# Performance work log

Measured on AMD Instinct MI355X. Metric: run time of the kernel, lower is better.

The kernel has to match this reference:

```python
import jax, jax.numpy as jnp
import numpy as np

M, N, D, P = 1024, 4096, 128, 2048
H = N // D  # 32
L = 4096   # cache length


def setup_inputs() -> dict:
    key = jax.random.key(0)
    ks = jax.random.split(key, 6)
    # scales keep the naive (non max-subtracted) exp-softmax in fp32 range
    X = jax.random.normal(ks[0], (M, N), dtype=jnp.float32) * 0.5
    W_q = jax.random.normal(ks[1], (N, N), dtype=jnp.float32) * 0.01
    W_k = jax.random.normal(ks[2], (N, N), dtype=jnp.float32) * 0.01
    W_v = jax.random.normal(ks[3], (N, N), dtype=jnp.float32) * 0.01
    cache_K = jax.random.normal(ks[4], (H, L, D), dtype=jnp.float32) * 0.1
    cache_V = jax.random.normal(ks[5], (H, L, D), dtype=jnp.float32) * 0.1
    return {"X": X, "W_q": W_q, "W_k": W_k, "W_v": W_v,
            "cache_K": cache_K, "cache_V": cache_V}


def reference(X, W_q, W_k, W_v, cache_K, cache_V):
    # fused QKV projection: [M, N] @ [N, 3N]
    W_qkv = jnp.concatenate([W_q, W_k, W_v], axis=1)
    qkv = X @ W_qkv
    q, k, v = jnp.split(qkv, 3, axis=-1)
    q = q.reshape(M, H, D).transpose(1, 0, 2)  # [H, M, D]
    k = k.reshape(M, H, D).transpose(1, 0, 2)  # [H, M, D]
    v = v.reshape(M, H, D).transpose(1, 0, 2)  # [H, M, D]
    # KV-cache write at position P
    k_cache = jax.lax.dynamic_update_slice(cache_K, k, (0, P, 0))  # [H, L, D]
    v_cache = jax.lax.dynamic_update_slice(cache_V, v, (0, P, 0))
    # naive (no max-subtraction) exp softmax attention over the full cache
    scores = jnp.einsum('hmd,hld->hml', q, k_cache)  # [H, M, L]
    scores_exp = jnp.exp(scores)
    weights = scores_exp / jnp.sum(scores_exp, axis=-1, keepdims=True)
    output = jnp.einsum('hml,hld->hmd', weights, v_cache)  # [H, M, D]
    return output.transpose(1, 0, 2).reshape(M, H * D)
```

## Files before the change

### kernel.cpp

```cpp
#include <hip/hip_runtime.h>

#define MM 1024
#define NN 4096
#define DD 128
#define HH 32
#define LL 4096
#define PP 2048

typedef __attribute__((ext_vector_type(8))) short short8;
typedef __attribute__((ext_vector_type(4))) float f32x4;

__device__ __forceinline__ ushort f2bf(float f) {
  unsigned u = __builtin_bit_cast(unsigned, f);
  u += 0x7fffu + ((u >> 16) & 1u);
  return (ushort)(u >> 16);
}

__device__ __forceinline__ void gl_lds16(const void* g, void* l) {
  __builtin_amdgcn_global_load_lds(
      (const __attribute__((address_space(1))) void*)g,
      (__attribute__((address_space(3))) void*)l, 16, 0, 0);
}

__global__ __launch_bounds__(256) void convert_kernel(
    const float* __restrict__ src, ushort* __restrict__ dst, int n8) {
  int i = blockIdx.x * 256 + threadIdx.x;
  if (i >= n8) return;
  const float4* s = (const float4*)src + (size_t)i * 2;
  float4 a = s[0], b = s[1];
  union { ushort s[8]; uint4 v; } pk;
  pk.s[0] = f2bf(a.x); pk.s[1] = f2bf(a.y);
  pk.s[2] = f2bf(a.z); pk.s[3] = f2bf(a.w);
  pk.s[4] = f2bf(b.x); pk.s[5] = f2bf(b.y);
  pk.s[6] = f2bf(b.z); pk.s[7] = f2bf(b.w);
  ((uint4*)dst)[i] = pk.v;
}

__global__ __launch_bounds__(256) void transpose_w_kernel(
    const float* __restrict__ W0, const float* __restrict__ W1,
    const float* __restrict__ W2, ushort* __restrict__ Wt) {
  __shared__ __align__(16) ushort tile[64][72];
  int z = blockIdx.z;
  const float* W = (z == 0) ? W0 : ((z == 1) ? W1 : W2);
  ushort* out = Wt + (size_t)z * NN * NN;
  int r0 = blockIdx.x * 64, c0 = blockIdx.y * 64;
  int t = threadIdx.x;
#pragma unroll
  for (int i = 0; i < 4; ++i) {
    int c = i * 256 + t;
    int r = c >> 4, cc = (c & 15) * 4;
    float4 v = *(const float4*)(W + (size_t)(r0 + r) * NN + c0 + cc);
    tile[r][cc + 0] = f2bf(v.x);
    tile[r][cc + 1] = f2bf(v.y);
    tile[r][cc + 2] = f2bf(v.z);
    tile[r][cc + 3] = f2bf(v.w);
  }
  __syncthreads();
#pragma unroll
  for (int i = 0; i < 2; ++i) {
    int c = i * 256 + t;
    int j = c >> 3, kk = (c & 7) * 8;
    union { ushort s[8]; uint4 v; } pk;
#pragma unroll
    for (int u = 0; u < 8; ++u) pk.s[u] = tile[kk + u][j];
    *(uint4*)(out + (size_t)(c0 + j) * NN + r0 + kk) = pk.v;
  }
}

__global__ __launch_bounds__(256) void transpose_v_kernel(
    const float* __restrict__ cacheV, const ushort* __restrict__ v_new,
    ushort* __restrict__ Vt) {
  __shared__ __align__(16) ushort tile[64][72];
  int l0 = blockIdx.x * 64, d0 = blockIdx.y * 64, h = blockIdx.z;
  int t = threadIdx.x;
  bool isnew = (l0 >= PP && l0 < PP + MM);
  if (isnew) {
    const ushort* src = v_new + (size_t)(l0 - PP) * NN + h * DD + d0;
#pragma unroll
    for (int i = 0; i < 2; ++i) {
      int c = i * 256 + t;
      int r = c >> 3, cc = (c & 7) * 8;
      *(uint4*)&tile[r][cc] = *(const uint4*)(src + (size_t)r * NN + cc);
    }
  } else {
    const float* src = cacheV + ((size_t)h * LL + l0) * DD + d0;
#pragma unroll
    for (int i = 0; i < 4; ++i) {
      int c = i * 256 + t;
      int r = c >> 4, cc = (c & 15) * 4;
      float4 v = *(const float4*)(src + (size_t)r * DD + cc);
      tile[r][cc + 0] = f2bf(v.x);
      tile[r][cc + 1] = f2bf(v.y);
      tile[r][cc + 2] = f2bf(v.z);
      tile[r][cc + 3] = f2bf(v.w);
    }
  }
  __syncthreads();
#pragma unroll
  for (int i = 0; i < 2; ++i) {
    int c = i * 256 + t;
    int j = c >> 3, kk = (c & 7) * 8;
    union { ushort s[8]; uint4 v; } pk;
#pragma unroll
    for (int u = 0; u < 8; ++u) pk.s[u] = tile[kk + u][j];
    *(uint4*)(Vt + ((size_t)(h * DD + d0 + j)) * LL + l0 + kk) = pk.v;
  }
}

__global__ __launch_bounds__(256) void qkv_gemm_kernel(
    const ushort* __restrict__ X, const ushort* __restrict__ Wt,
    ushort* __restrict__ q_ws, ushort* __restrict__ k_ws,
    ushort* __restrict__ v_ws) {
  __shared__ __align__(16) ushort Alds[128 * 64];
  __shared__ __align__(16) ushort Blds[128 * 64];
  int t = threadIdx.x;
  int lane = t & 63, quad = lane >> 4, l15 = lane & 15;
  int wv = t >> 6, wm = wv >> 1, wn = wv & 1;
  int m0 = blockIdx.x * 128;
  int wsel = blockIdx.y >> 5;
  int col0 = (blockIdx.y & 31) * 128;
  const ushort* Wsrc = Wt + (size_t)wsel * NN * NN + (size_t)col0 * NN;
  ushort* dst = (wsel == 0) ? q_ws : ((wsel == 1) ? k_ws : v_ws);

  int wuni = __builtin_amdgcn_readfirstlane(t & 192);

  const ushort* aG[4];
  const ushort* bG[4];
  unsigned ldsb[4];
#pragma unroll
  for (int i = 0; i < 4; ++i) {
    int c = i * 256 + t;
    int row = c >> 3, g = (c & 7) ^ (row & 7);
    aG[i] = X + (size_t)(m0 + row) * NN + g * 8;
    bG[i] = Wsrc + (size_t)row * NN + g * 8;
    ldsb[i] = (unsigned)(i * 256 + wuni) * 16u;
  }
  unsigned aAddr[4][2], bAddr[4][2];
#pragma unroll
  for (int mb = 0; mb < 4; ++mb)
#pragma unroll
    for (int s = 0; s < 2; ++s) {
      int row = wm * 64 + mb * 16 + l15;
      int g = s * 4 + quad;
      aAddr[mb][s] = (unsigned)(row * 128 + ((g ^ (row & 7)) * 16));
    }
#pragma unroll
  for (int nb = 0; nb < 4; ++nb)
#pragma unroll
    for (int s = 0; s < 2; ++s) {
      int row = wn * 64 + nb * 16 + l15;
      int g = s * 4 + quad;
      bAddr[nb][s] = (unsigned)(row * 128 + ((g ^ (row & 7)) * 16));
    }

  f32x4 acc[4][4];
#pragma unroll
  for (int mb = 0; mb < 4; ++mb)
#pragma unroll
    for (int nb = 0; nb < 4; ++nb) acc[mb][nb] = (f32x4){0.f, 0.f, 0.f, 0.f};

  for (int kt = 0; kt < 64; ++kt) {
#pragma unroll
    for (int i = 0; i < 4; ++i) gl_lds16(aG[i], (char*)Alds + ldsb[i]);
#pragma unroll
    for (int i = 0; i < 4; ++i) gl_lds16(bG[i], (char*)Blds + ldsb[i]);
#pragma unroll
    for (int i = 0; i < 4; ++i) { aG[i] += 64; bG[i] += 64; }
    __syncthreads();
#pragma unroll
    for (int s = 0; s < 2; ++s) {
      short8 af[4], bf[4];
#pragma unroll
      for (int mb = 0; mb < 4; ++mb)
        af[mb] = *(const short8*)((const char*)Alds + aAddr[mb][s]);
#pragma unroll
      for (int nb = 0; nb < 4; ++nb)
        bf[nb] = *(const short8*)((const char*)Blds + bAddr[nb][s]);
#pragma unroll
      for (int mb = 0; mb < 4; ++mb)
#pragma unroll
        for (int nb = 0; nb < 4; ++nb)
          acc[mb][nb] = __builtin_amdgcn_mfma_f32_16x16x32_bf16(
              af[mb], bf[nb], acc[mb][nb], 0, 0, 0);
    }
    __syncthreads();
  }

#pragma unroll
  for (int mb = 0; mb < 4; ++mb)
#pragma unroll
    for (int nb = 0; nb < 4; ++nb)
#pragma unroll
      for (int r = 0; r < 4; ++r) {
        int row = m0 + wm * 64 + mb * 16 + quad * 4 + r;
        int col = col0 + wn * 64 + nb * 16 + l15;
        dst[(size_t)row * NN + col] = f2bf(acc[mb][nb][r]);
      }
}

__global__ __launch_bounds__(256) void attn_kernel(
    const ushort* __restrict__ q_ws, const ushort* __restrict__ k_ws,
    const ushort* __restrict__ Kb, const ushort* __restrict__ Vt,
    float* __restrict__ out) {
  __shared__ __align__(16) char smem[42240];
  float* denlds = (float*)(smem + 41984);
  float* Olds = (float*)smem;

  int t = threadIdx.x;
  int lane = t & 63, quad = lane >> 4, l15 = lane & 15;
  int wv = t >> 6;
  int h = blockIdx.y, m0 = blockIdx.x * 64;
  int wuni = __builtin_amdgcn_readfirstlane(t & 192);

  short8 qf[4];
  {
    const ushort* qrow =
        q_ws + (size_t)(m0 + wv * 16 + l15) * NN + h * DD + quad * 8;
#pragma unroll
    for (int s = 0; s < 4; ++s) qf[s] = *(const short8*)(qrow + s * 32);
  }

  int kRow[4], kOff[4];
  unsigned kLb[4];
  const ushort* vG[4];
  unsigned vLb[4];
#pragma unroll
  for (int i = 0; i < 4; ++i) {
    int c = i * 256 + t;
    int krow = c >> 4, kg = (c & 15) ^ (krow & 15);
    kRow[i] = krow; kOff[i] = kg * 8;
    kLb[i] = (unsigned)(i * 256 + wuni) * 16u;
    int vrow = c >> 3, vg = (c & 7) ^ (vrow & 7);
    vG[i] = Vt + ((size_t)(h * DD + vrow)) * LL + vg * 8;
    vLb[i] = 16384u + (unsigned)(i * 256 + wuni) * 16u;
  }
  unsigned kAddr[4][4], vAddr[2][2], pAddr[2][4];
#pragma unroll
  for (int lb = 0; lb < 4; ++lb)
#pragma unroll
    for (int ds = 0; ds < 4; ++ds) {
      int l = lb * 16 + l15, g = ds * 4 + quad;
      kAddr[lb][ds] = (unsigned)(l * 256 + ((g ^ l15) * 16));
    }
#pragma unroll
  for (int ls = 0; ls < 2; ++ls)
#pragma unroll
    for (int db = 0; db < 2; ++db) {
      int d = wv * 32 + db * 16 + l15, g = ls * 4 + quad;
      vAddr[ls][db] = 16384u + (unsigned)(d * 128 + ((g ^ (l15 & 7)) * 16));
    }
#pragma unroll
  for (int ls = 0; ls < 2; ++ls)
#pragma unroll
    for (int mb = 0; mb < 4; ++mb)
      pAddr[ls][mb] =
          32768u + (unsigned)((mb * 16 + l15) * 144 + ls * 64 + quad * 16);

  f32x4 Oacc[2][4];
#pragma unroll
  for (int db = 0; db < 2; ++db)
#pragma unroll
    for (int mb = 0; mb < 4; ++mb) Oacc[db][mb] = (f32x4){0.f, 0.f, 0.f, 0.f};
  float denp[4] = {0.f, 0.f, 0.f, 0.f};

  for (int lt = 0; lt < 64; ++lt) {
    int l0 = lt * 64;
    const ushort* ksrc;
    size_t kstride;
    if (l0 >= PP && l0 < PP + MM) {
      ksrc = k_ws + (size_t)(l0 - PP) * NN + h * DD;
      kstride = NN;
    } else {
      ksrc = Kb + ((size_t)h * LL + l0) * DD;
      kstride = DD;
    }
    __syncthreads();
#pragma unroll
    for (int i = 0; i < 4; ++i)
      gl_lds16(ksrc + (size_t)kRow[i] * kstride + kOff[i], smem + kLb[i]);
#pragma unroll
    for (int i = 0; i < 4; ++i) {
      gl_lds16(vG[i], smem + vLb[i]);
      vG[i] += 64;
    }
    __syncthreads();

#pragma unroll
    for (int lb = 0; lb < 4; ++lb) {
      f32x4 s = (f32x4){0.f, 0.f, 0.f, 0.f};
#pragma unroll
      for (int ds = 0; ds < 4; ++ds) {
        short8 bk = *(const short8*)(smem + kAddr[lb][ds]);
        s = __builtin_amdgcn_mfma_f32_16x16x32_bf16(qf[ds], bk, s, 0, 0, 0);
      }
#pragma unroll
      for (int r = 0; r < 4; ++r) {
        float e = __expf(s[r]);
        denp[r] += e;
        *(ushort*)(smem + 32768 + (wv * 16 + quad * 4 + r) * 144 +
                   (lb * 16 + l15) * 2) = f2bf(e);
      }
    }
    __syncthreads();

#pragma unroll
    for (int ls = 0; ls < 2; ++ls) {
      short8 av0 = *(const short8*)(smem + vAddr[ls][0]);
      short8 av1 = *(const short8*)(smem + vAddr[ls][1]);
#pragma unroll
      for (int mb = 0; mb < 4; ++mb) {
        short8 bp = *(const short8*)(smem + pAddr[ls][mb]);
        Oacc[0][mb] =
            __builtin_amdgcn_mfma_f32_16x16x32_bf16(av0, bp, Oacc[0][mb], 0, 0, 0);
        Oacc[1][mb] =
            __builtin_amdgcn_mfma_f32_16x16x32_bf16(av1, bp, Oacc[1][mb], 0, 0, 0);
      }
    }
  }

  __syncthreads();
#pragma unroll
  for (int r = 0; r < 4; ++r) {
    float v = denp[r];
    v += __shfl_xor(v, 1);
    v += __shfl_xor(v, 2);
    v += __shfl_xor(v, 4);
    v += __shfl_xor(v, 8);
    denp[r] = v;
  }
  if (l15 == 0) {
#pragma unroll
    for (int r = 0; r < 4; ++r) denlds[wv * 16 + quad * 4 + r] = denp[r];
  }
  __syncthreads();

#pragma unroll
  for (int mb = 0; mb < 4; ++mb) {
    float inv = 1.0f / denlds[mb * 16 + l15];
#pragma unroll
    for (int db = 0; db < 2; ++db)
#pragma unroll
      for (int r = 0; r < 4; ++r) {
        int d = wv * 32 + db * 16 + quad * 4 + r;
        Olds[(mb * 16 + l15) * 136 + d] = Oacc[db][mb][r] * inv;
      }
  }
  __syncthreads();
  {
    int m = t >> 2, c0 = (t & 3) * 32;
    float* orow = out + (size_t)(m0 + m) * NN + h * DD + c0;
#pragma unroll
    for (int j = 0; j < 32; j += 4) {
      float4 v;
      v.x = Olds[m * 136 + c0 + j + 0];
      v.y = Olds[m * 136 + c0 + j + 1];
      v.z = Olds[m * 136 + c0 + j + 2];
      v.w = Olds[m * 136 + c0 + j + 3];
      *(float4*)(orow + j) = v;
    }
  }
}

extern "C" void kernel_launch(void* const* d_in, const int* in_sizes, int n_in,
                              void* d_out, int out_size, void* d_ws,
                              size_t ws_size, hipStream_t stream) {
  const float* X = (const float*)d_in[0];
  const float* Wq = (const float*)d_in[1];
  const float* Wk = (const float*)d_in[2];
  const float* Wv = (const float*)d_in[3];
  const float* cK = (const float*)d_in[4];
  const float* cV = (const float*)d_in[5];
  float* out = (float*)d_out;
  char* wsb = (char*)d_ws;

  ushort* Wt = (ushort*)wsb;
  ushort* Kb = (ushort*)wsb;
  ushort* Vt = (ushort*)(wsb + 33554432);
  ushort* Xb = (ushort*)(wsb + 100663296);
  ushort* q_ws = (ushort*)(wsb + 109051904);
  ushort* k_ws = (ushort*)(wsb + 117440512);
  ushort* v_ws = (ushort*)(wsb + 125829120);

  convert_kernel<<<2048, 256, 0, stream>>>(X, Xb, MM * NN / 8);
  transpose_w_kernel<<<dim3(64, 64, 3), 256, 0, stream>>>(Wq, Wk, Wv, Wt);
  qkv_gemm_kernel<<<dim3(8, 96), 256, 0, stream>>>(Xb, Wt, q_ws, k_ws, v_ws);
  convert_kernel<<<8192, 256, 0, stream>>>(cK, Kb, HH * LL * DD / 8);
  transpose_v_kernel<<<dim3(64, 2, 32), 256, 0, stream>>>(cV, v_ws, Vt);
  attn_kernel<<<dim3(16, 32), 256, 0, stream>>>(q_ws, k_ws, Kb, Vt, out);
}
```

Measured before the change: 566.2 us.

## Double-buffer K tiles with manual vmcnt waits and remap attention block indices

Adds a second LDS buffer for K so the next tile's K load is issued while the current tile is being computed. Replaces __syncthreads with explicit s_waitcnt vmcnt counts plus s_barrier, and raises wave priority around the MFMA sections. It also swizzles the block-to-(head, m-tile) mapping so concurrently scheduled blocks share heads differently, aiming for better cache locality. LDS use grows, which may lower occupancy, and hand-counted vmcnt values are fragile if the compiler reorders memory ops.

Result: no change. 564.6 us, median of 2 (-0.3%).

```diff
diff --git a/kernel.cpp b/kernel.cpp
--- a/kernel.cpp
+++ b/kernel.cpp
@@ -202,14 +202,17 @@
     const ushort* __restrict__ q_ws, const ushort* __restrict__ k_ws,
     const ushort* __restrict__ Kb, const ushort* __restrict__ Vt,
     float* __restrict__ out) {
-  __shared__ __align__(16) char smem[42240];
-  float* denlds = (float*)(smem + 41984);
+  __shared__ __align__(16) char smem[58624];
+  float* denlds = (float*)(smem + 58368);
   float* Olds = (float*)smem;
 
   int t = threadIdx.x;
   int lane = t & 63, quad = lane >> 4, l15 = lane & 15;
   int wv = t >> 6;
-  int h = blockIdx.y, m0 = blockIdx.x * 64;
+  int flat = (int)(blockIdx.y * 16 + blockIdx.x);
+  int swz = ((flat & 7) << 6) | (flat >> 3);
+  int m0 = (swz & 15) * 64;
+  int h = swz >> 4;
   int wuni = __builtin_amdgcn_readfirstlane(t & 192);
 
   short8 qf[4];
@@ -232,7 +235,7 @@
     kLb[i] = (unsigned)(i * 256 + wuni) * 16u;
     int vrow = c >> 3, vg = (c & 7) ^ (vrow & 7);
     vG[i] = Vt + ((size_t)(h * DD + vrow)) * LL + vg * 8;
-    vLb[i] = 16384u + (unsigned)(i * 256 + wuni) * 16u;
+    vLb[i] = 32768u + (unsigned)(i * 256 + wuni) * 16u;
   }
   unsigned kAddr[4][4], vAddr[2][2], pAddr[2][4];
 #pragma unroll
@@ -247,14 +250,14 @@
 #pragma unroll
     for (int db = 0; db < 2; ++db) {
       int d = wv * 32 + db * 16 + l15, g = ls * 4 + quad;
-      vAddr[ls][db] = 16384u + (unsigned)(d * 128 + ((g ^ (l15 & 7)) * 16));
+      vAddr[ls][db] = 32768u + (unsigned)(d * 128 + ((g ^ (l15 & 7)) * 16));
     }
 #pragma unroll
   for (int ls = 0; ls < 2; ++ls)
 #pragma unroll
     for (int mb = 0; mb < 4; ++mb)
       pAddr[ls][mb] =
-          32768u + (unsigned)((mb * 16 + l15) * 144 + ls * 64 + quad * 16);
+          49152u + (unsigned)((mb * 16 + l15) * 144 + ls * 64 + quad * 16);
 
   f32x4 Oacc[2][4];
 #pragma unroll
@@ -263,46 +266,70 @@
     for (int mb = 0; mb < 4; ++mb) Oacc[db][mb] = (f32x4){0.f, 0.f, 0.f, 0.f};
   float denp[4] = {0.f, 0.f, 0.f, 0.f};
 
+  {
+    const ushort* ks = Kb + (size_t)h * LL * DD;
+#pragma unroll
+    for (int i = 0; i < 4; ++i)
+      gl_lds16(ks + (size_t)kRow[i] * DD + kOff[i], smem + kLb[i]);
+  }
+
   for (int lt = 0; lt < 64; ++lt) {
-    int l0 = lt * 64;
-    const ushort* ksrc;
-    size_t kstride;
-    if (l0 >= PP && l0 < PP + MM) {
-      ksrc = k_ws + (size_t)(l0 - PP) * NN + h * DD;
-      kstride = NN;
-    } else {
-      ksrc = Kb + ((size_t)h * LL + l0) * DD;
-      kstride = DD;
-    }
-    __syncthreads();
-#pragma unroll
-    for (int i = 0; i < 4; ++i)
-      gl_lds16(ksrc + (size_t)kRow[i] * kstride + kOff[i], smem + kLb[i]);
+    unsigned krd = (unsigned)(lt & 1) << 14;
+    if (lt < 63) {
+      int l0n = (lt + 1) * 64;
+      const ushort* ks2;
+      size_t kst2;
+      if (l0n >= PP && l0n < PP + MM) {
+        ks2 = k_ws + (size_t)(l0n - PP) * NN + h * DD;
+        kst2 = NN;
+      } else {
+        ks2 = Kb + ((size_t)h * LL + l0n) * DD;
+        kst2 = DD;
+      }
+      unsigned kb = krd ^ 16384u;
+#pragma unroll
+      for (int i = 0; i < 4; ++i)
+        gl_lds16(ks2 + (size_t)kRow[i] * kst2 + kOff[i], smem + kb + kLb[i]);
+    }
 #pragma unroll
     for (int i = 0; i < 4; ++i) {
       gl_lds16(vG[i], smem + vLb[i]);
       vG[i] += 64;
     }
-    __syncthreads();
-
+    if (lt < 63)
+      asm volatile("s_waitcnt vmcnt(8)" ::: "memory");
+    else
+      asm volatile("s_waitcnt vmcnt(4)" ::: "memory");
+    __builtin_amdgcn_s_barrier();
+    asm volatile("" ::: "memory");
+
+    __builtin_amdgcn_s_setprio(1);
 #pragma unroll
     for (int lb = 0; lb < 4; ++lb) {
       f32x4 s = (f32x4){0.f, 0.f, 0.f, 0.f};
 #pragma unroll
       for (int ds = 0; ds < 4; ++ds) {
-        short8 bk = *(const short8*)(smem + kAddr[lb][ds]);
+        short8 bk = *(const short8*)(smem + krd + kAddr[lb][ds]);
         s = __builtin_amdgcn_mfma_f32_16x16x32_bf16(qf[ds], bk, s, 0, 0, 0);
       }
 #pragma unroll
       for (int r = 0; r < 4; ++r) {
         float e = __expf(s[r]);
         denp[r] += e;
-        *(ushort*)(smem + 32768 + (wv * 16 + quad * 4 + r) * 144 +
+        *(ushort*)(smem + 49152 + (wv * 16 + quad * 4 + r) * 144 +
                    (lb * 16 + l15) * 2) = f2bf(e);
       }
     }
-    __syncthreads();
-
+    __builtin_amdgcn_s_setprio(0);
+
+    if (lt < 63)
+      asm volatile("s_waitcnt vmcnt(4) lgkmcnt(0)" ::: "memory");
+    else
+      asm volatile("s_waitcnt vmcnt(0) lgkmcnt(0)" ::: "memory");
+    __builtin_amdgcn_s_barrier();
+    asm volatile("" ::: "memory");
+
+    __builtin_amdgcn_s_setprio(1);
 #pragma unroll
     for (int ls = 0; ls < 2; ++ls) {
       short8 av0 = *(const short8*)(smem + vAddr[ls][0]);
@@ -316,6 +343,11 @@
             __builtin_amdgcn_mfma_f32_16x16x32_bf16(av1, bp, Oacc[1][mb], 0, 0, 0);
       }
     }
+    __builtin_amdgcn_s_setprio(0);
+
+    asm volatile("" ::: "memory");
+    __builtin_amdgcn_s_barrier();
+    asm volatile("" ::: "memory");
   }
 
   __syncthreads();
```

## Restructure attention kernel with register-prefetched K/V and per-wave key split

Applied to the files above, without the earlier changes.

Rewrites the attention loop so each wave owns a 16-key slice of each 64-key tile for all 64 query rows, instead of a 16-row query slice over all keys. K and V fragments are loaded straight from global memory into registers and double-buffered, prefetching the next tile while the current one computes. Only the P tile goes through LDS, which shrinks shared memory and allows two blocks per CU. It also adds MFMA priority hints, block-index swizzling, and a cross-wave denominator reduction. The costs are more registers (all Q fragments held per wave) and uncoalesced per-lane global loads of K/V.

Result: slower. 579.5 us (+2.4%).

```diff
diff --git a/kernel.cpp b/kernel.cpp
--- a/kernel.cpp
+++ b/kernel.cpp
@@ -198,151 +198,164 @@
       }
 }
 
-__global__ __launch_bounds__(256) void attn_kernel(
+__global__ __launch_bounds__(256, 2) void attn_kernel(
     const ushort* __restrict__ q_ws, const ushort* __restrict__ k_ws,
     const ushort* __restrict__ Kb, const ushort* __restrict__ Vt,
     float* __restrict__ out) {
-  __shared__ __align__(16) char smem[42240];
-  float* denlds = (float*)(smem + 41984);
+  __shared__ __align__(16) char smem[35840];
+  ushort* Plds = (ushort*)smem;
+  float* denlds = (float*)(smem + 34816);
   float* Olds = (float*)smem;
 
   int t = threadIdx.x;
   int lane = t & 63, quad = lane >> 4, l15 = lane & 15;
   int wv = t >> 6;
-  int h = blockIdx.y, m0 = blockIdx.x * 64;
-  int wuni = __builtin_amdgcn_readfirstlane(t & 192);
-
-  short8 qf[4];
+  int quad8 = quad * 8, quad4 = quad * 4, wv16 = wv * 16;
+  int wv16l15 = wv16 + l15;
+  int flat = (int)(blockIdx.y * 16 + blockIdx.x);
+  int swz = ((flat & 7) << 6) | (flat >> 3);
+  int m0 = (swz & 15) * 64;
+  int h = swz >> 4;
+
+  short8 qf[4][4];
+#pragma unroll
+  for (int mb = 0; mb < 4; ++mb) {
+    const ushort* qr =
+        q_ws + (size_t)(m0 + mb * 16 + l15) * NN + h * DD + quad8;
+#pragma unroll
+    for (int ds = 0; ds < 4; ++ds) qf[mb][ds] = *(const short8*)(qr + ds * 32);
+  }
+
+  const ushort* vrow = Vt + ((size_t)(h * DD + wv * 32 + l15)) * LL;
+  const ushort* vrow16 = vrow + (size_t)16 * LL;
+
+  f32x4 Oacc[2][4];
+#pragma unroll
+  for (int db = 0; db < 2; ++db)
+#pragma unroll
+    for (int mb = 0; mb < 4; ++mb) Oacc[db][mb] = (f32x4){0.f, 0.f, 0.f, 0.f};
+  float denp[4][4];
+#pragma unroll
+  for (int mb = 0; mb < 4; ++mb)
+#pragma unroll
+    for (int r = 0; r < 4; ++r) denp[mb][r] = 0.f;
+
+  short8 kra[4], krb[4], vra[2][2], vrb[2][2];
+
   {
-    const ushort* qrow =
-        q_ws + (size_t)(m0 + wv * 16 + l15) * NN + h * DD + quad * 8;
-#pragma unroll
-    for (int s = 0; s < 4; ++s) qf[s] = *(const short8*)(qrow + s * 32);
-  }
-
-  int kRow[4], kOff[4];
-  unsigned kLb[4];
-  const ushort* vG[4];
-  unsigned vLb[4];
-#pragma unroll
-  for (int i = 0; i < 4; ++i) {
-    int c = i * 256 + t;
-    int krow = c >> 4, kg = (c & 15) ^ (krow & 15);
-    kRow[i] = krow; kOff[i] = kg * 8;
-    kLb[i] = (unsigned)(i * 256 + wuni) * 16u;
-    int vrow = c >> 3, vg = (c & 7) ^ (vrow & 7);
-    vG[i] = Vt + ((size_t)(h * DD + vrow)) * LL + vg * 8;
-    vLb[i] = 16384u + (unsigned)(i * 256 + wuni) * 16u;
-  }
-  unsigned kAddr[4][4], vAddr[2][2], pAddr[2][4];
-#pragma unroll
-  for (int lb = 0; lb < 4; ++lb)
-#pragma unroll
-    for (int ds = 0; ds < 4; ++ds) {
-      int l = lb * 16 + l15, g = ds * 4 + quad;
-      kAddr[lb][ds] = (unsigned)(l * 256 + ((g ^ l15) * 16));
-    }
-#pragma unroll
-  for (int ls = 0; ls < 2; ++ls)
-#pragma unroll
-    for (int db = 0; db < 2; ++db) {
-      int d = wv * 32 + db * 16 + l15, g = ls * 4 + quad;
-      vAddr[ls][db] = 16384u + (unsigned)(d * 128 + ((g ^ (l15 & 7)) * 16));
-    }
-#pragma unroll
-  for (int ls = 0; ls < 2; ++ls)
+    const ushort* kp = Kb + ((size_t)h * LL + wv16l15) * DD;
+    kra[0] = *(const short8*)(kp + quad8);
+    kra[1] = *(const short8*)(kp + 32 + quad8);
+    kra[2] = *(const short8*)(kp + 64 + quad8);
+    kra[3] = *(const short8*)(kp + 96 + quad8);
+    vra[0][0] = *(const short8*)(vrow + quad8);
+    vra[0][1] = *(const short8*)(vrow + 32 + quad8);
+    vra[1][0] = *(const short8*)(vrow16 + quad8);
+    vra[1][1] = *(const short8*)(vrow16 + 32 + quad8);
+  }
+
+#define ATTN_STEP(LT, KC, VC, KN, VN, PF)                                      \
+  do {                                                                         \
+    if (PF) {          \
+      int l0n = ((LT) + 1) << 6;                                               \
+      size_t krow = (size_t)l0n + (size_t)wv16l15;                             \
+      const ushort* kp = (l0n >= PP && l0n < PP + MM)                          \
+                             ? k_ws + (krow - PP) * NN + h * DD                \
+                             : Kb + ((size_t)h * LL + krow) * DD;              \
+      KN[0] = *(const short8*)(kp + quad8);                                    \
+      KN[1] = *(const short8*)(kp + 32 + quad8);                               \
+      KN[2] = *(const short8*)(kp + 64 + quad8);                               \
+      KN[3] = *(const short8*)(kp + 96 + quad8);                               \
+      const ushort* vp0 = vrow + l0n;                                          \
+      const ushort* vp1 = vrow16 + l0n;                                        \
+      VN[0][0] = *(const short8*)(vp0 + quad8);                                \
+      VN[0][1] = *(const short8*)(vp0 + 32 + quad8);                           \
+      VN[1][0] = *(const short8*)(vp1 + quad8);                                \
+      VN[1][1] = *(const short8*)(vp1 + 32 + quad8);                           \
+    }                                                                          \
+      \
+    f32x4 sac[4];                                                              \
+    __builtin_amdgcn_s_setprio(1);                                             \
+    _Pragma("unroll") for (int mb = 0; mb < 4; ++mb) {                         \
+      f32x4 s = (f32x4){0.f, 0.f, 0.f, 0.f};                                   \
+      s = __builtin_amdgcn_mfma_f32_16x16x32_bf16(qf[mb][0], KC[0], s, 0, 0, 0);\
+      s = __builtin_amdgcn_mfma_f32_16x16x32_bf16(qf[mb][1], KC[1], s, 0, 0, 0);\
+      s = __builtin_amdgcn_mfma_f32_16x16x32_bf16(qf[mb][2], KC[2], s, 0, 0, 0);\
+      s = __builtin_amdgcn_mfma_f32_16x16x32_bf16(qf[mb][3], KC[3], s, 0, 0, 0);\
+      sac[mb] = s;                                                             \
+    }                                                                          \
+    __builtin_amdgcn_s_setprio(0);                                             \
+    _Pragma("unroll") for (int mb = 0; mb < 4; ++mb) {                         \
+      float e0 = __expf(sac[mb][0]), e1 = __expf(sac[mb][1]);                  \
+      float e2 = __expf(sac[mb][2]), e3 = __expf(sac[mb][3]);                  \
+      denp[mb][0] += e0; denp[mb][1] += e1;                                    \
+      denp[mb][2] += e2; denp[mb][3] += e3;                                    \
+      ushort* pw = Plds + (mb * 16 + quad4) * 72 + wv16l15;                    \
+      pw[0] = f2bf(e0); pw[72] = f2bf(e1);                                     \
+      pw[144] = f2bf(e2); pw[216] = f2bf(e3);                                  \
+    }                                                                          \
+    asm volatile("s_waitcnt lgkmcnt(0)" ::: "memory");                         \
+    __builtin_amdgcn_s_barrier();     \
+          \
+    __builtin_amdgcn_s_setprio(1);                                             \
+    _Pragma("unroll") for (int mb = 0; mb < 4; ++mb) {                         \
+      const ushort* pr = Plds + (mb * 16 + l15) * 72 + quad8;                  \
+      short8 p0 = *(const short8*)pr;                                          \
+      short8 p1 = *(const short8*)(pr + 32);                                   \
+      Oacc[0][mb] = __builtin_amdgcn_mfma_f32_16x16x32_bf16(VC[0][0], p0,      \
+                                                            Oacc[0][mb], 0, 0, 0);\
+      Oacc[0][mb] = __builtin_amdgcn_mfma_f32_16x16x32_bf16(VC[0][1], p1,      \
+                                                            Oacc[0][mb], 0, 0, 0);\
+      Oacc[1][mb] = __builtin_amdgcn_mfma_f32_16x16x32_bf16(VC[1][0], p0,      \
+                                                            Oacc[1][mb], 0, 0, 0);\
+      Oacc[1][mb] = __builtin_amdgcn_mfma_f32_16x16x32_bf16(VC[1][1], p1,      \
+                                                            Oacc[1][mb], 0, 0, 0);\
+    }                                                                          \
+    __builtin_amdgcn_s_setprio(0);                                             \
+    asm volatile("s_waitcnt lgkmcnt(0)" ::: "memory");                         \
+    __builtin_amdgcn_s_barrier();   \
+  } while (0)
+
+  for (int i = 0; i < 31; ++i) {
+    ATTN_STEP(2 * i, kra, vra, krb, vrb, 1);
+    ATTN_STEP(2 * i + 1, krb, vrb, kra, vra, 1);
+  }
+  ATTN_STEP(62, kra, vra, krb, vrb, 1);
+  ATTN_STEP(63, krb, vrb, kra, vra, 0);
+#undef ATTN_STEP
+
+#pragma unroll
+  for (int mb = 0; mb < 4; ++mb)
+#pragma unroll
+    for (int r = 0; r < 4; ++r) {
+      float v = denp[mb][r];
+      v += __shfl_xor(v, 1);
+      v += __shfl_xor(v, 2);
+      v += __shfl_xor(v, 4);
+      v += __shfl_xor(v, 8);
+      denp[mb][r] = v;
+    }
+  if (l15 == 0) {
 #pragma unroll
     for (int mb = 0; mb < 4; ++mb)
-      pAddr[ls][mb] =
-          32768u + (unsigned)((mb * 16 + l15) * 144 + ls * 64 + quad * 16);
-
-  f32x4 Oacc[2][4];
-#pragma unroll
-  for (int db = 0; db < 2; ++db)
-#pragma unroll
-    for (int mb = 0; mb < 4; ++mb) Oacc[db][mb] = (f32x4){0.f, 0.f, 0.f, 0.f};
-  float denp[4] = {0.f, 0.f, 0.f, 0.f};
-
-  for (int lt = 0; lt < 64; ++lt) {
-    int l0 = lt * 64;
-    const ushort* ksrc;
-    size_t kstride;
-    if (l0 >= PP && l0 < PP + MM) {
-      ksrc = k_ws + (size_t)(l0 - PP) * NN + h * DD;
-      kstride = NN;
-    } else {
-      ksrc = Kb + ((size_t)h * LL + l0) * DD;
-      kstride = DD;
-    }
-    __syncthreads();
-#pragma unroll
-    for (int i = 0; i < 4; ++i)
-      gl_lds16(ksrc + (size_t)kRow[i] * kstride + kOff[i], smem + kLb[i]);
-#pragma unroll
-    for (int i = 0; i < 4; ++i) {
-      gl_lds16(vG[i], smem + vLb[i]);
-      vG[i] += 64;
-    }
-    __syncthreads();
-
-#pragma unroll
-    for (int lb = 0; lb < 4; ++lb) {
-      f32x4 s = (f32x4){0.f, 0.f, 0.f, 0.f};
-#pragma unroll
-      for (int ds = 0; ds < 4; ++ds) {
-        short8 bk = *(const short8*)(smem + kAddr[lb][ds]);
-        s = __builtin_amdgcn_mfma_f32_16x16x32_bf16(qf[ds], bk, s, 0, 0, 0);
-      }
+#pragma unroll
+      for (int r = 0; r < 4; ++r)
+        denlds[wv * 64 + mb * 16 + quad4 + r] = denp[mb][r];
+  }
+  __syncthreads();
+
+#pragma unroll
+  for (int mb = 0; mb < 4; ++mb) {
+    int m = mb * 16 + l15;
+    float den =
+        denlds[m] + denlds[64 + m] + denlds[128 + m] + denlds[192 + m];
+    float inv = 1.0f / den;
+#pragma unroll
+    for (int db = 0; db < 2; ++db)
 #pragma unroll
       for (int r = 0; r < 4; ++r) {
-        float e = __expf(s[r]);
-        denp[r] += e;
-        *(ushort*)(smem + 32768 + (wv * 16 + quad * 4 + r) * 144 +
-                   (lb * 16 + l15) * 2) = f2bf(e);
-      }
-    }
-    __syncthreads();
-
-#pragma unroll
-    for (int ls = 0; ls < 2; ++ls) {
-      short8 av0 = *(const short8*)(smem + vAddr[ls][0]);
-      short8 av1 = *(const short8*)(smem + vAddr[ls][1]);
-#pragma unroll
-      for (int mb = 0; mb < 4; ++mb) {
-        short8 bp = *(const short8*)(smem + pAddr[ls][mb]);
-        Oacc[0][mb] =
-            __builtin_amdgcn_mfma_f32_16x16x32_bf16(av0, bp, Oacc[0][mb], 0, 0, 0);
-        Oacc[1][mb] =
-            __builtin_amdgcn_mfma_f32_16x16x32_bf16(av1, bp, Oacc[1][mb], 0, 0, 0);
-      }
-    }
-  }
-
-  __syncthreads();
-#pragma unroll
-  for (int r = 0; r < 4; ++r) {
-    float v = denp[r];
-    v += __shfl_xor(v, 1);
-    v += __shfl_xor(v, 2);
-    v += __shfl_xor(v, 4);
-    v += __shfl_xor(v, 8);
-    denp[r] = v;
-  }
-  if (l15 == 0) {
-#pragma unroll
-    for (int r = 0; r < 4; ++r) denlds[wv * 16 + quad * 4 + r] = denp[r];
-  }
-  __syncthreads();
-
-#pragma unroll
-  for (int mb = 0; mb < 4; ++mb) {
-    float inv = 1.0f / denlds[mb * 16 + l15];
-#pragma unroll
-    for (int db = 0; db < 2; ++db)
-#pragma unroll
-      for (int r = 0; r < 4; ++r) {
-        int d = wv * 32 + db * 16 + quad * 4 + r;
-        Olds[(mb * 16 + l15) * 136 + d] = Oacc[db][mb][r] * inv;
+        int d = wv * 32 + db * 16 + quad4 + r;
+        Olds[m * 136 + d] = Oacc[db][mb][r] * inv;
       }
   }
   __syncthreads();
```
